# Kernel tuning notes

Measured on AMD Instinct MI355X. Metric: run time of the kernel, lower is better.

Reference implementation:

```python
import jax, jax.numpy as jnp
import numpy as np

N_ENT = 50000
N_REL = 16
N_BASES = 8
H_DIM = 128
N_EDGES = 800000


def setup_inputs() -> dict:
    key = jax.random.key(0)
    ks = jax.random.split(key, 12)
    s = 1.0 / np.sqrt(H_DIM)
    inp = {
        "entity_emb": jax.random.normal(ks[0], (N_ENT, H_DIM), jnp.float32) * s,
        "basis1": jax.random.normal(ks[1], (N_BASES, H_DIM, H_DIM), jnp.float32) * s,
        "w_comp1": jax.random.normal(ks[2], (N_REL, N_BASES), jnp.float32) * (1.0 / np.sqrt(N_BASES)),
        "loop_w1": jax.random.normal(ks[3], (H_DIM, H_DIM), jnp.float32) * s,
        "bias1": jnp.zeros((H_DIM,), jnp.float32),
        "basis2": jax.random.normal(ks[4], (N_BASES, H_DIM, H_DIM), jnp.float32) * s,
        "w_comp2": jax.random.normal(ks[5], (N_REL, N_BASES), jnp.float32) * (1.0 / np.sqrt(N_BASES)),
        "loop_w2": jax.random.normal(ks[6], (H_DIM, H_DIM), jnp.float32) * s,
        "bias2": jnp.zeros((H_DIM,), jnp.float32),
        "src": jax.random.randint(ks[7], (N_EDGES,), 0, N_ENT, jnp.int32),
        "dst": jax.random.randint(ks[8], (N_EDGES,), 0, N_ENT, jnp.int32),
        "rel_type": jax.random.randint(ks[9], (N_EDGES,), 0, N_REL, jnp.int32),
    }
    return inp


def _rgcn_layer(h, src, dst, rel, basis, w_comp, loop_w, bias):
    # Basis decomposition: W_r = sum_b w_comp[r, b] * basis[b]   -> [R, d, d]
    W = jnp.einsum('rb,bio->rio', w_comp, basis)
    # Sum aggregation is linear, so aggregate h[src] per (dst, rel) first,
    # then apply the relation matrix once per (node, rel). Same math as
    # per-edge transform + scatter-add, far less FLOP/traffic.
    seg = dst.astype(jnp.int32) * N_REL + rel.astype(jnp.int32)  # [E]
    agg = jax.ops.segment_sum(h[src], seg, num_segments=N_ENT * N_REL)
    agg = agg.reshape(N_ENT, N_REL, -1)                           # [N, R, d]
    msg = jnp.einsum('nri,rio->no', agg, W)                       # [N, d]
    out = msg + h @ loop_w + bias
    return jax.nn.relu(out)


def reference(entity_emb, basis1, w_comp1, loop_w1, bias1,
              basis2, w_comp2, loop_w2, bias2, src, dst, rel_type):
    # Encoder dropout is identity in eval mode.
    h = _rgcn_layer(entity_emb, src, dst, rel_type, basis1, w_comp1, loop_w1, bias1)
    h = _rgcn_layer(h, src, dst, rel_type, basis2, w_comp2, loop_w2, bias2)
    return h
```

## Files before the change

### kernel.cpp

```cpp
#include <hip/hip_runtime.h>
#include <hip/hip_bf16.h>

#define HDIM 128
#define NREL 16
#define NBASES 8
#define KSLOTS 17
#define KDIM (KSLOTS * HDIM)
#define LDSA 136

typedef short bf16x8 __attribute__((ext_vector_type(8)));
typedef short s16x4 __attribute__((ext_vector_type(4)));
typedef float f32x4 __attribute__((ext_vector_type(4)));

static __device__ __forceinline__ short f2bf(float x) {
    __hip_bfloat16 b = __float2bfloat16(x);
    return *(short*)&b;
}
static __device__ __forceinline__ float bf2f(short u) {
    unsigned v = ((unsigned)(unsigned short)u) << 16;
    return __uint_as_float(v);
}

__global__ void compute_wt(const float* __restrict__ basis,
                           const float* __restrict__ wcomp,
                           short* __restrict__ wtL) {
    int ro = blockIdx.x;
    int r = ro >> 7, o = ro & 127;
    int i = threadIdx.x;
    float acc = 0.f;
#pragma unroll
    for (int b = 0; b < NBASES; ++b)
        acc += wcomp[r * NBASES + b] * basis[(b * HDIM + i) * HDIM + o];
    wtL[(size_t)o * KDIM + r * HDIM + i] = f2bf(acc);
}

__global__ void transposeL(const float* __restrict__ in, short* __restrict__ wtL) {
    int o = blockIdx.x, i = threadIdx.x;
    wtL[(size_t)o * KDIM + NREL * HDIM + i] = f2bf(in[i * HDIM + o]);
}

__global__ void cast_bf16(const float* __restrict__ in, short* __restrict__ out, int n4) {
    for (int i = blockIdx.x * blockDim.x + threadIdx.x; i < n4; i += gridDim.x * blockDim.x) {
        f32x4 v = ((const f32x4*)in)[i];
        s16x4 o;
#pragma unroll
        for (int j = 0; j < 4; ++j) o[j] = f2bf(v[j]);
        ((s16x4*)out)[i] = o;
    }
}

__global__ void zero_i32(int* __restrict__ p, int n) {
    int i = blockIdx.x * blockDim.x + threadIdx.x;
    if (i < n) p[i] = 0;
}

__global__ __launch_bounds__(256) void hist_k(const int* __restrict__ dst,
                                              const int* __restrict__ rel, int n,
                                              int* __restrict__ hist) {
    for (int i = blockIdx.x * blockDim.x + threadIdx.x; i < n; i += gridDim.x * blockDim.x)
        atomicAdd(&hist[dst[i] * NREL + rel[i]], 1);
}

__global__ __launch_bounds__(1024) void scan_p1(const int* __restrict__ hist, int n,
                                                int* __restrict__ off, int* __restrict__ part) {
    __shared__ int sh[1024];
    int t = threadIdx.x, b = blockIdx.x;
    int i = b * 1024 + t;
    int x = (i < n) ? hist[i] : 0;
    sh[t] = x;
    __syncthreads();
    for (int d = 1; d < 1024; d <<= 1) {
        int v = sh[t];
        int u = (t >= d) ? sh[t - d] : 0;
        __syncthreads();
        sh[t] = v + u;
        __syncthreads();
    }
    if (i < n) off[i] = sh[t] - x;
    if (t == 1023) part[b] = sh[t];
}

__global__ __launch_bounds__(1024) void scan_p2(int* __restrict__ part, int nb) {
    __shared__ int sh[1024];
    int t = threadIdx.x;
    int x = (t < nb) ? part[t] : 0;
    sh[t] = x;
    __syncthreads();
    for (int d = 1; d < 1024; d <<= 1) {
        int v = sh[t];
        int u = (t >= d) ? sh[t - d] : 0;
        __syncthreads();
        sh[t] = v + u;
        __syncthreads();
    }
    if (t < nb) part[t] = sh[t] - x;
}

__global__ __launch_bounds__(1024) void scan_p3(int* __restrict__ off, const int* __restrict__ part,
                                                int n, int nk, int* __restrict__ cur) {
    int i = blockIdx.x * 1024 + threadIdx.x;
    if (i < n) {
        int v = off[i] + part[blockIdx.x];
        off[i] = v;
        if (i < nk) cur[i] = v;
    }
}

__global__ __launch_bounds__(256) void scatter_k(const int* __restrict__ src,
                                                 const int* __restrict__ dst,
                                                 const int* __restrict__ rel, int n,
                                                 int* __restrict__ cur,
                                                 int* __restrict__ edge2) {
    for (int i = blockIdx.x * blockDim.x + threadIdx.x; i < n; i += gridDim.x * blockDim.x) {
        int k = dst[i] * NREL + rel[i];
        int p = atomicAdd(&cur[k], 1);
        edge2[p] = (src[i] & 0xFFFF) | (rel[i] << 16);
    }
}

__global__ __launch_bounds__(256) void agg_build(
    const short* __restrict__ h,
    const int* __restrict__ off,
    const int* __restrict__ edge2,
    short* __restrict__ AGG,
    unsigned char* __restrict__ mask,
    int c0, int rows) {
    int tid = threadIdx.x;
    int grp = blockIdx.x * 16 + (tid >> 4);
    int lane16 = tid & 15;
    int lane = tid & 63;
    int gb = lane & 48;
    int drow = grp >> 1;
    if (drow >= rows) return;
    int rh = (grp & 1) * 8;
    int d = c0 + drow;
    int kbase = d * NREL + rh;

    int e0 = off[kbase];
    int e1 = off[kbase + 8];
    int deg = e1 - e0;

    int pkv = (e0 + lane16 < e1) ? edge2[e0 + lane16] : 0;

    bf16x8 va[16];
    int rlv[16];
#pragma unroll
    for (int p = 0; p < 16; ++p) {
        int pk = __shfl(pkv, gb + p);
        rlv[p] = ((pk >> 16) & 15) - rh;
        const short* hp = h + (size_t)(pk & 0xFFFF) * HDIM + lane16 * 8;
        if (p < deg) va[p] = *(const bf16x8*)hp;
    }

    float acc[8];
    int cs = -1;
    unsigned mbits = 0;
    short* outp = AGG + ((size_t)drow * NREL + rh) * HDIM + lane16 * 8;

    auto emit = [&]() {
        bf16x8 o;
#pragma unroll
        for (int c = 0; c < 8; ++c) o[c] = f2bf(acc[c]);
        *(bf16x8*)(outp + cs * HDIM) = o;
        mbits |= 1u << cs;
    };
    auto take = [&](int sl, bf16x8 v) {
        if (sl != cs) {
            if (cs >= 0) emit();
            cs = sl;
#pragma unroll
            for (int c = 0; c < 8; ++c) acc[c] = 0.f;
        }
#pragma unroll
        for (int c = 0; c < 8; ++c) acc[c] += bf2f(v[c]);
    };

#pragma unroll
    for (int p = 0; p < 16; ++p)
        if (p < deg) take(rlv[p], va[p]);

    for (int e = e0 + 16; e < e1; ++e) {
        int pk = edge2[e];
        bf16x8 v = *(const bf16x8*)(h + (size_t)(pk & 0xFFFF) * HDIM + lane16 * 8);
        take(((pk >> 16) & 15) - rh, v);
    }
    if (cs >= 0) emit();

    if (lane16 == 0) mask[(size_t)drow * 2 + (rh >> 3)] = (unsigned char)mbits;
}

__global__ __launch_bounds__(256, 3) void agg_gemm(
    const short* __restrict__ AGG,
    const short* __restrict__ h,
    const short* __restrict__ wtL,
    const unsigned char* __restrict__ mask,
    const float* __restrict__ bias,
    short* __restrict__ out_bf,
    float* __restrict__ out_f,
    int c0, int rows) {
    __shared__ short As[64 * LDSA];
    __shared__ short Bs[128 * LDSA];
    int tid = threadIdx.x;
    int row0 = blockIdx.x * 64;
    if (row0 >= rows) return;
    int wave = tid >> 6, lane = tid & 63;
    int mq = (wave & 1) * 32, nq = (wave >> 1) * 64;
    int lr = lane & 15, quad = lane >> 4;

    int r2 = tid >> 2, ch = (tid & 3) * 32;
    int rb = tid >> 1, hb = (tid & 1) * 64;
    bool ok = (row0 + r2) < rows;
    unsigned mk = ok ? *(const unsigned short*)(mask + (size_t)(row0 + r2) * 2) : 0;

    bf16x8 apf[4], bpf[8];

    auto loadRegs = [&](int ks) {
        const short* bp = wtL + (size_t)rb * KDIM + ks * HDIM + hb;
#pragma unroll
        for (int j = 0; j < 8; ++j) bpf[j] = *(const bf16x8*)(bp + j * 8);
        if (ks == 16) {
            const short* sp = h + (size_t)(c0 + row0 + r2) * HDIM + ch;
#pragma unroll
            for (int j = 0; j < 4; ++j) apf[j] = ok ? *(const bf16x8*)(sp + j * 8) : (bf16x8)0;
        } else if (ok && ((mk >> ks) & 1)) {
            const short* sp = AGG + ((size_t)(row0 + r2) * NREL + ks) * HDIM + ch;
#pragma unroll
            for (int j = 0; j < 4; ++j) apf[j] = *(const bf16x8*)(sp + j * 8);
        } else {
#pragma unroll
            for (int j = 0; j < 4; ++j) apf[j] = (bf16x8)0;
        }
    };
    auto writeLDS = [&]() {
        short* ad = As + r2 * LDSA + ch;
#pragma unroll
        for (int j = 0; j < 4; ++j) *(bf16x8*)(ad + j * 8) = apf[j];
        short* bd = Bs + rb * LDSA + hb;
#pragma unroll
        for (int j = 0; j < 8; ++j) *(bf16x8*)(bd + j * 8) = bpf[j];
    };

    f32x4 acc[2][4] = {};

    loadRegs(0);
    writeLDS();
    __syncthreads();

#pragma unroll 1
    for (int ks = 0; ks <= 16; ++ks) {
        if (ks < 16) loadRegs(ks + 1);
#pragma unroll
        for (int kk = 0; kk < 4; ++kk) {
            int kb = kk * 32 + quad * 8;
            bf16x8 a[2], b[4];
#pragma unroll
            for (int mi = 0; mi < 2; ++mi)
                a[mi] = *(const bf16x8*)(As + (mq + mi * 16 + lr) * LDSA + kb);
#pragma unroll
            for (int ni = 0; ni < 4; ++ni)
                b[ni] = *(const bf16x8*)(Bs + (nq + ni * 16 + lr) * LDSA + kb);
#pragma unroll
            for (int mi = 0; mi < 2; ++mi)
#pragma unroll
                for (int ni = 0; ni < 4; ++ni)
                    acc[mi][ni] = __builtin_amdgcn_mfma_f32_16x16x32_bf16(a[mi], b[ni], acc[mi][ni], 0, 0, 0);
        }
        __syncthreads();
        if (ks < 16) { writeLDS(); __syncthreads(); }
    }

#pragma unroll
    for (int mi = 0; mi < 2; ++mi) {
#pragma unroll
        for (int reg = 0; reg < 4; ++reg) {
            int g = row0 + mq + mi * 16 + quad * 4 + reg;
            if (g < rows) {
                size_t gd = (size_t)(c0 + g) * HDIM;
#pragma unroll
                for (int ni = 0; ni < 4; ++ni) {
                    int n = nq + ni * 16 + lr;
                    float v = acc[mi][ni][reg] + bias[n];
                    v = v > 0.f ? v : 0.f;
                    if (out_bf) out_bf[gd + n] = f2bf(v);
                    else        out_f[gd + n] = v;
                }
            }
        }
    }
}

extern "C" void kernel_launch(void* const* d_in, const int* in_sizes, int n_in,
                              void* d_out, int out_size, void* d_ws, size_t ws_size,
                              hipStream_t stream) {
    const float* emb    = (const float*)d_in[0];
    const float* basis1 = (const float*)d_in[1];
    const float* wc1    = (const float*)d_in[2];
    const float* lw1    = (const float*)d_in[3];
    const float* bias1  = (const float*)d_in[4];
    const float* basis2 = (const float*)d_in[5];
    const float* wc2    = (const float*)d_in[6];
    const float* lw2    = (const float*)d_in[7];
    const float* bias2  = (const float*)d_in[8];
    const int* src = (const int*)d_in[9];
    const int* dst = (const int*)d_in[10];
    const int* rel = (const int*)d_in[11];

    int n_ent = in_sizes[0] / HDIM;
    int n_edges = in_sizes[9];
    int NK = n_ent * NREL;
    int NK1 = NK + 1;

    char* ws = (char*)d_ws;
    size_t wo = 0;
    auto alloc = [&](size_t bytes) {
        void* p = ws + wo;
        wo = (wo + bytes + 255) & ~(size_t)255;
        return p;
    };
    int* hist  = (int*)alloc((size_t)NK1 * 4);
    int* off   = (int*)alloc((size_t)NK1 * 4);
    int* cur   = (int*)alloc((size_t)NK * 4);
    int* part  = (int*)alloc(4096);
    int* edge2 = (int*)alloc((size_t)n_edges * 4);
    short* wtL1 = (short*)alloc((size_t)HDIM * KDIM * 2);
    short* wtL2 = (short*)alloc((size_t)HDIM * KDIM * 2);
    short* h0   = (short*)alloc((size_t)n_ent * HDIM * 2);
    short* h1   = (short*)alloc((size_t)n_ent * HDIM * 2);
    unsigned char* mask = (unsigned char*)alloc((size_t)n_ent * 2);

    size_t rowBytes = (size_t)NREL * HDIM * 2;
    size_t avail = (ws_size > wo + rowBytes * 128) ? (ws_size - wo) : rowBytes * 128;
    int CH = (int)(avail / rowBytes);
    if (CH > n_ent) CH = n_ent;
    CH = (CH + 127) & ~127;
    if (CH < 128) CH = 128;
    while ((size_t)CH * rowBytes > avail && CH > 128) CH -= 128;
    short* AGG = (short*)alloc((size_t)CH * rowBytes);

    compute_wt<<<NREL * HDIM, HDIM, 0, stream>>>(basis1, wc1, wtL1);
    compute_wt<<<NREL * HDIM, HDIM, 0, stream>>>(basis2, wc2, wtL2);
    transposeL<<<HDIM, HDIM, 0, stream>>>(lw1, wtL1);
    transposeL<<<HDIM, HDIM, 0, stream>>>(lw2, wtL2);
    cast_bf16<<<512, 256, 0, stream>>>(emb, h0, n_ent * HDIM / 4);

    zero_i32<<<(NK1 + 255) / 256, 256, 0, stream>>>(hist, NK1);
    hist_k<<<1024, 256, 0, stream>>>(dst, rel, n_edges, hist);
    int nsb = (NK1 + 1023) / 1024;
    scan_p1<<<nsb, 1024, 0, stream>>>(hist, NK1, off, part);
    scan_p2<<<1, 1024, 0, stream>>>(part, nsb);
    scan_p3<<<nsb, 1024, 0, stream>>>(off, part, NK1, NK, cur);
    scatter_k<<<1024, 256, 0, stream>>>(src, dst, rel, n_edges, cur, edge2);

    for (int c0 = 0; c0 < n_ent; c0 += CH) {
        int rows = n_ent - c0 < CH ? n_ent - c0 : CH;
        agg_build<<<(rows * 2 + 15) / 16, 256, 0, stream>>>(h0, off, edge2, AGG, mask, c0, rows);
        agg_gemm<<<(rows + 63) / 64, 256, 0, stream>>>(AGG, h0, wtL1, mask, bias1,
                                                       h1, nullptr, c0, rows);
    }
    for (int c0 = 0; c0 < n_ent; c0 += CH) {
        int rows = n_ent - c0 < CH ? n_ent - c0 : CH;
        agg_build<<<(rows * 2 + 15) / 16, 256, 0, stream>>>(h1, off, edge2, AGG, mask, c0, rows);
        agg_gemm<<<(rows + 63) / 64, 256, 0, stream>>>(AGG, h1, wtL2, mask, bias2,
                                                       nullptr, (float*)d_out, c0, rows);
    }
}
```

Before: 502.3 us.

## Skip materializing single-edge aggregates; read source rows directly in GEMM, swizzle LDS

agg_build now detects (dst, rel) slots that hold exactly one edge and, instead of summing and writing them to AGG, records the source node index in a per-slot srcs array. Multi-edge slots are marked with a sentinel and still go through AGG, and empty slots get a different sentinel. agg_gemm reads the slot descriptor and loads the A tile either from AGG, directly from h, or as zeros. This cuts AGG write and read traffic, since most slots in the random graph have degree one. The padded LDS layout is also replaced with an XOR-swizzled unpadded layout to avoid bank conflicts, which adds index arithmetic and a larger per-row srcs array.

```diff
diff --git a/kernel.cpp b/kernel.cpp
--- a/kernel.cpp
+++ b/kernel.cpp
@@ -6,7 +6,6 @@
 #define NBASES 8
 #define KSLOTS 17
 #define KDIM (KSLOTS * HDIM)
-#define LDSA 136
 
 typedef short bf16x8 __attribute__((ext_vector_type(8)));
 typedef short s16x4 __attribute__((ext_vector_type(4)));
@@ -123,7 +122,7 @@
     const int* __restrict__ off,
     const int* __restrict__ edge2,
     short* __restrict__ AGG,
-    unsigned char* __restrict__ mask,
+    unsigned short* __restrict__ srcs,
     int c0, int rows) {
     int tid = threadIdx.x;
     int grp = blockIdx.x * 16 + (tid >> 4);
@@ -137,24 +136,39 @@
     int kbase = d * NREL + rh;
 
     int e0 = off[kbase];
-    int e1 = off[kbase + 8];
-    int deg = e1 - e0;
-
-    int pkv = (e0 + lane16 < e1) ? edge2[e0 + lane16] : 0;
-
-    bf16x8 va[16];
-    int rlv[16];
+    int e8 = off[kbase + 8];
+    int deg = e8 - e0;
+
+    int pkv = (e0 + lane16 < e8) ? edge2[e0 + lane16] : 0;
+
+    int rlv[17], srcv[16];
 #pragma unroll
     for (int p = 0; p < 16; ++p) {
         int pk = __shfl(pkv, gb + p);
-        rlv[p] = ((pk >> 16) & 15) - rh;
-        const short* hp = h + (size_t)(pk & 0xFFFF) * HDIM + lane16 * 8;
-        if (p < deg) va[p] = *(const bf16x8*)hp;
-    }
-
-    float acc[8];
+        rlv[p] = (p < deg) ? (((pk >> 16) & 15) - rh) : 255;
+        srcv[p] = pk & 0xFFFF;
+    }
+    rlv[16] = (deg > 16) ? rlv[15] : 255;
+
+    bool single[16];
+#pragma unroll
+    for (int p = 0; p < 16; ++p)
+        single[p] = ((p == 0) || (rlv[p - 1] != rlv[p])) && (rlv[p + 1] != rlv[p]);
+
+    bf16x8 va[16];
+#pragma unroll
+    for (int p = 0; p < 16; ++p)
+        if (p < deg && !single[p])
+            va[p] = *(const bf16x8*)(h + (size_t)srcv[p] * HDIM + lane16 * 8);
+
+    unsigned short val = 0xFFFF;
+#pragma unroll
+    for (int p = 0; p < 16; ++p)
+        if (p < deg && rlv[p] == lane16)
+            val = single[p] ? (unsigned short)srcv[p] : (unsigned short)0xFFFE;
+
+    float acc[8] = {0.f, 0.f, 0.f, 0.f, 0.f, 0.f, 0.f, 0.f};
     int cs = -1;
-    unsigned mbits = 0;
     short* outp = AGG + ((size_t)drow * NREL + rh) * HDIM + lane16 * 8;
 
     auto emit = [&]() {
@@ -162,7 +176,6 @@
 #pragma unroll
         for (int c = 0; c < 8; ++c) o[c] = f2bf(acc[c]);
         *(bf16x8*)(outp + cs * HDIM) = o;
-        mbits |= 1u << cs;
     };
     auto take = [&](int sl, bf16x8 v) {
         if (sl != cs) {
@@ -177,29 +190,31 @@
 
 #pragma unroll
     for (int p = 0; p < 16; ++p)
-        if (p < deg) take(rlv[p], va[p]);
-
-    for (int e = e0 + 16; e < e1; ++e) {
+        if (p < deg && !single[p]) take(rlv[p], va[p]);
+
+    for (int e = e0 + 16; e < e8; ++e) {
         int pk = edge2[e];
+        int sl = ((pk >> 16) & 15) - rh;
+        if (sl == lane16) val = 0xFFFE;
         bf16x8 v = *(const bf16x8*)(h + (size_t)(pk & 0xFFFF) * HDIM + lane16 * 8);
-        take(((pk >> 16) & 15) - rh, v);
+        take(sl, v);
     }
     if (cs >= 0) emit();
 
-    if (lane16 == 0) mask[(size_t)drow * 2 + (rh >> 3)] = (unsigned char)mbits;
+    if (lane16 < 8) srcs[(size_t)drow * NREL + rh + lane16] = val;
 }
 
 __global__ __launch_bounds__(256, 3) void agg_gemm(
     const short* __restrict__ AGG,
     const short* __restrict__ h,
     const short* __restrict__ wtL,
-    const unsigned char* __restrict__ mask,
+    const unsigned short* __restrict__ srcs,
     const float* __restrict__ bias,
     short* __restrict__ out_bf,
     float* __restrict__ out_f,
     int c0, int rows) {
-    __shared__ short As[64 * LDSA];
-    __shared__ short Bs[128 * LDSA];
+    __shared__ short As[64 * HDIM];
+    __shared__ short Bs[128 * HDIM];
     int tid = threadIdx.x;
     int row0 = blockIdx.x * 64;
     if (row0 >= rows) return;
@@ -207,37 +222,64 @@
     int mq = (wave & 1) * 32, nq = (wave >> 1) * 64;
     int lr = lane & 15, quad = lane >> 4;
 
-    int r2 = tid >> 2, ch = (tid & 3) * 32;
-    int rb = tid >> 1, hb = (tid & 1) * 64;
+    int r2 = tid >> 2, ca = tid & 3;
+    int rb = tid >> 1, cb = (tid & 1) * 8;
     bool ok = (row0 + r2) < rows;
-    unsigned mk = ok ? *(const unsigned short*)(mask + (size_t)(row0 + r2) * 2) : 0;
+
+    unsigned wq[8];
+    {
+        uint4 a = make_uint4(0xFFFFFFFFu, 0xFFFFFFFFu, 0xFFFFFFFFu, 0xFFFFFFFFu);
+        uint4 b = a;
+        if (ok) {
+            const uint4* sp = (const uint4*)(srcs + (size_t)(row0 + r2) * NREL);
+            a = sp[0]; b = sp[1];
+        }
+        wq[0] = a.x; wq[1] = a.y; wq[2] = a.z; wq[3] = a.w;
+        wq[4] = b.x; wq[5] = b.y; wq[6] = b.z; wq[7] = b.w;
+    }
 
     bf16x8 apf[4], bpf[8];
-
     auto loadRegs = [&](int ks) {
-        const short* bp = wtL + (size_t)rb * KDIM + ks * HDIM + hb;
+        const short* bp = wtL + (size_t)rb * KDIM + ks * HDIM + cb * 8;
 #pragma unroll
         for (int j = 0; j < 8; ++j) bpf[j] = *(const bf16x8*)(bp + j * 8);
         if (ks == 16) {
-            const short* sp = h + (size_t)(c0 + row0 + r2) * HDIM + ch;
-#pragma unroll
-            for (int j = 0; j < 4; ++j) apf[j] = ok ? *(const bf16x8*)(sp + j * 8) : (bf16x8)0;
-        } else if (ok && ((mk >> ks) & 1)) {
-            const short* sp = AGG + ((size_t)(row0 + r2) * NREL + ks) * HDIM + ch;
-#pragma unroll
-            for (int j = 0; j < 4; ++j) apf[j] = *(const bf16x8*)(sp + j * 8);
+            if (ok) {
+                const short* sp = h + (size_t)(c0 + row0 + r2) * HDIM + ca * 32;
+#pragma unroll
+                for (int j = 0; j < 4; ++j) apf[j] = *(const bf16x8*)(sp + j * 8);
+            } else {
+#pragma unroll
+                for (int j = 0; j < 4; ++j) apf[j] = (bf16x8)0;
+            }
         } else {
-#pragma unroll
-            for (int j = 0; j < 4; ++j) apf[j] = (bf16x8)0;
+            unsigned w = 0xFFFFu;
+#pragma unroll
+            for (int q = 0; q < 8; ++q) if ((ks >> 1) == q) w = wq[q];
+            unsigned e = (ks & 1) ? (w >> 16) : (w & 0xFFFFu);
+            if (e == 0xFFFFu) {
+#pragma unroll
+                for (int j = 0; j < 4; ++j) apf[j] = (bf16x8)0;
+            } else {
+                const short* sp = (e == 0xFFFEu)
+                    ? AGG + ((size_t)(row0 + r2) * NREL + ks) * HDIM + ca * 32
+                    : h + (size_t)e * HDIM + ca * 32;
+#pragma unroll
+                for (int j = 0; j < 4; ++j) apf[j] = *(const bf16x8*)(sp + j * 8);
+            }
         }
     };
     auto writeLDS = [&]() {
-        short* ad = As + r2 * LDSA + ch;
-#pragma unroll
-        for (int j = 0; j < 4; ++j) *(bf16x8*)(ad + j * 8) = apf[j];
-        short* bd = Bs + rb * LDSA + hb;
-#pragma unroll
-        for (int j = 0; j < 8; ++j) *(bf16x8*)(bd + j * 8) = bpf[j];
+#pragma unroll
+        for (int j = 0; j < 4; ++j) {
+            int c = ca * 4 + j;
+            *(bf16x8*)(As + r2 * HDIM + (c ^ (r2 & 7)) * 8) = apf[j];
+        }
+#pragma unroll
+        for (int j = 0; j < 8; ++j) {
+            int c = cb + j;
+            *(bf16x8*)(Bs + rb * HDIM + (c ^ (rb & 7)) * 8) = bpf[j];
+        }
     };
 
     f32x4 acc[2][4] = {};
@@ -251,14 +293,18 @@
         if (ks < 16) loadRegs(ks + 1);
 #pragma unroll
         for (int kk = 0; kk < 4; ++kk) {
-            int kb = kk * 32 + quad * 8;
+            int c = kk * 4 + quad;
             bf16x8 a[2], b[4];
 #pragma unroll
-            for (int mi = 0; mi < 2; ++mi)
-                a[mi] = *(const bf16x8*)(As + (mq + mi * 16 + lr) * LDSA + kb);
-#pragma unroll
-            for (int ni = 0; ni < 4; ++ni)
-                b[ni] = *(const bf16x8*)(Bs + (nq + ni * 16 + lr) * LDSA + kb);
+            for (int mi = 0; mi < 2; ++mi) {
+                int row = mq + mi * 16 + lr;
+                a[mi] = *(const bf16x8*)(As + row * HDIM + (c ^ (row & 7)) * 8);
+            }
+#pragma unroll
+            for (int ni = 0; ni < 4; ++ni) {
+                int row = nq + ni * 16 + lr;
+                b[ni] = *(const bf16x8*)(Bs + row * HDIM + (c ^ (row & 7)) * 8);
+            }
 #pragma unroll
             for (int mi = 0; mi < 2; ++mi)
 #pragma unroll
@@ -326,7 +372,7 @@
     short* wtL2 = (short*)alloc((size_t)HDIM * KDIM * 2);
     short* h0   = (short*)alloc((size_t)n_ent * HDIM * 2);
     short* h1   = (short*)alloc((size_t)n_ent * HDIM * 2);
-    unsigned char* mask = (unsigned char*)alloc((size_t)n_ent * 2);
+    unsigned short* srcs = (unsigned short*)alloc((size_t)n_ent * NREL * 2);
 
     size_t rowBytes = (size_t)NREL * HDIM * 2;
     size_t avail = (ws_size > wo + rowBytes * 128) ? (ws_size - wo) : rowBytes * 128;
@@ -353,14 +399,14 @@
 
     for (int c0 = 0; c0 < n_ent; c0 += CH) {
         int rows = n_ent - c0 < CH ? n_ent - c0 : CH;
-        agg_build<<<(rows * 2 + 15) / 16, 256, 0, stream>>>(h0, off, edge2, AGG, mask, c0, rows);
-        agg_gemm<<<(rows + 63) / 64, 256, 0, stream>>>(AGG, h0, wtL1, mask, bias1,
+        agg_build<<<(rows * 2 + 15) / 16, 256, 0, stream>>>(h0, off, edge2, AGG, srcs, c0, rows);
+        agg_gemm<<<(rows + 63) / 64, 256, 0, stream>>>(AGG, h0, wtL1, srcs, bias1,
                                                        h1, nullptr, c0, rows);
     }
     for (int c0 = 0; c0 < n_ent; c0 += CH) {
         int rows = n_ent - c0 < CH ? n_ent - c0 : CH;
-        agg_build<<<(rows * 2 + 15) / 16, 256, 0, stream>>>(h1, off, edge2, AGG, mask, c0, rows);
-        agg_gemm<<<(rows + 63) / 64, 256, 0, stream>>>(AGG, h1, wtL2, mask, bias2,
+        agg_build<<<(rows * 2 + 15) / 16, 256, 0, stream>>>(h1, off, edge2, AGG, srcs, c0, rows);
+        agg_gemm<<<(rows + 63) / 64, 256, 0, stream>>>(AGG, h1, wtL2, srcs, bias2,
                                                        nullptr, (float*)d_out, c0, rows);
     }
 }
```

Result: faster. 490.8 us (-2.3%).

## Compact aggregation buffer: store only multi-edge segments, reference single-edge sources directly

Applied to the files above, without the earlier changes.

Replaces the dense per-(node,relation) AGG buffer with a compacted buffer holding only segments of degree two or more, indexed through a second thresholded prefix scan. Single-edge segments store the source node index so the GEMM loads the h row directly, and empty segments are marked so their A tile is zeroed. This shrinks AGG write and read traffic and removes the chunked loop over entities, at the cost of an extra scan pass and indirect per-slot address selection in the GEMM.

```diff
diff --git a/kernel.cpp b/kernel.cpp
--- a/kernel.cpp
+++ b/kernel.cpp
@@ -62,11 +62,13 @@
 }
 
 __global__ __launch_bounds__(1024) void scan_p1(const int* __restrict__ hist, int n,
-                                                int* __restrict__ off, int* __restrict__ part) {
+                                                int* __restrict__ off, int* __restrict__ part,
+                                                int thr) {
     __shared__ int sh[1024];
     int t = threadIdx.x, b = blockIdx.x;
     int i = b * 1024 + t;
     int x = (i < n) ? hist[i] : 0;
+    if (thr) x = (x >= thr) ? 1 : 0;
     sh[t] = x;
     __syncthreads();
     for (int d = 1; d < 1024; d <<= 1) {
@@ -121,10 +123,11 @@
 __global__ __launch_bounds__(256) void agg_build(
     const short* __restrict__ h,
     const int* __restrict__ off,
+    const int* __restrict__ off2m,
     const int* __restrict__ edge2,
-    short* __restrict__ AGG,
-    unsigned char* __restrict__ mask,
-    int c0, int rows) {
+    short* __restrict__ AGGc,
+    unsigned* __restrict__ srcs,
+    int rows) {
     int tid = threadIdx.x;
     int grp = blockIdx.x * 16 + (tid >> 4);
     int lane16 = tid & 15;
@@ -133,36 +136,56 @@
     int drow = grp >> 1;
     if (drow >= rows) return;
     int rh = (grp & 1) * 8;
-    int d = c0 + drow;
-    int kbase = d * NREL + rh;
-
-    int e0 = off[kbase];
-    int e1 = off[kbase + 8];
-    int deg = e1 - e0;
-
-    int pkv = (e0 + lane16 < e1) ? edge2[e0 + lane16] : 0;
-
-    bf16x8 va[16];
-    int rlv[16];
+    int kbase = drow * NREL + rh;
+
+    int offv = (lane16 < 9) ? off[kbase + lane16] : 0;
+    int cmv  = (lane16 < 8) ? off2m[kbase + lane16] : 0;
+    int e0 = __shfl(offv, gb);
+    int e8 = __shfl(offv, gb + 8);
+    int deg = e8 - e0;
+    int nl = gb + ((lane16 < 8) ? lane16 + 1 : 0);
+    int degS = __shfl(offv, nl) - offv;
+
+    int pkv = (e0 + lane16 < e8) ? edge2[e0 + lane16] : 0;
+    int rlv[16], srcv[16], mul[16];
 #pragma unroll
     for (int p = 0; p < 16; ++p) {
         int pk = __shfl(pkv, gb + p);
-        rlv[p] = ((pk >> 16) & 15) - rh;
-        const short* hp = h + (size_t)(pk & 0xFFFF) * HDIM + lane16 * 8;
-        if (p < deg) va[p] = *(const bf16x8*)hp;
-    }
-
-    float acc[8];
+        int sl = ((pk >> 16) & 15) - rh;
+        rlv[p] = (p < deg) ? sl : 0;
+        srcv[p] = pk & 0xFFFF;
+        int ds = __shfl(degS, gb + rlv[p]);
+        mul[p] = (p < deg) && (ds >= 2);
+    }
+
+    bf16x8 va[16];
+#pragma unroll
+    for (int p = 0; p < 16; ++p)
+        if (mul[p])
+            va[p] = *(const bf16x8*)(h + (size_t)srcv[p] * HDIM + lane16 * 8);
+
+    unsigned val = 0xFFFFFFFFu;
+    if (lane16 < 8) {
+        if (degS >= 2) val = 0x80000000u | (unsigned)cmv;
+        else if (degS == 1) {
+            int ps = offv - e0;
+            if (ps < 16) {
+#pragma unroll
+                for (int p = 0; p < 16; ++p) if (ps == p) val = (unsigned)srcv[p];
+            } else {
+                val = (unsigned)(edge2[e0 + ps] & 0xFFFF);
+            }
+        }
+    }
+
+    float acc[8] = {0.f, 0.f, 0.f, 0.f, 0.f, 0.f, 0.f, 0.f};
     int cs = -1;
-    unsigned mbits = 0;
-    short* outp = AGG + ((size_t)drow * NREL + rh) * HDIM + lane16 * 8;
-
     auto emit = [&]() {
+        int cmS = __shfl(cmv, gb + cs);
         bf16x8 o;
 #pragma unroll
         for (int c = 0; c < 8; ++c) o[c] = f2bf(acc[c]);
-        *(bf16x8*)(outp + cs * HDIM) = o;
-        mbits |= 1u << cs;
+        *(bf16x8*)(AGGc + (size_t)cmS * HDIM + lane16 * 8) = o;
     };
     auto take = [&](int sl, bf16x8 v) {
         if (sl != cs) {
@@ -177,27 +200,31 @@
 
 #pragma unroll
     for (int p = 0; p < 16; ++p)
-        if (p < deg) take(rlv[p], va[p]);
-
-    for (int e = e0 + 16; e < e1; ++e) {
+        if (mul[p]) take(rlv[p], va[p]);
+
+    for (int e = e0 + 16; e < e8; ++e) {
         int pk = edge2[e];
-        bf16x8 v = *(const bf16x8*)(h + (size_t)(pk & 0xFFFF) * HDIM + lane16 * 8);
-        take(((pk >> 16) & 15) - rh, v);
+        int sl = ((pk >> 16) & 15) - rh;
+        int ds = __shfl(degS, gb + sl);
+        if (ds >= 2) {
+            bf16x8 v = *(const bf16x8*)(h + (size_t)(pk & 0xFFFF) * HDIM + lane16 * 8);
+            take(sl, v);
+        }
     }
     if (cs >= 0) emit();
 
-    if (lane16 == 0) mask[(size_t)drow * 2 + (rh >> 3)] = (unsigned char)mbits;
+    if (lane16 < 8) srcs[(size_t)drow * NREL + rh + lane16] = val;
 }
 
 __global__ __launch_bounds__(256, 3) void agg_gemm(
-    const short* __restrict__ AGG,
+    const short* __restrict__ AGGc,
     const short* __restrict__ h,
     const short* __restrict__ wtL,
-    const unsigned char* __restrict__ mask,
+    const unsigned* __restrict__ srcs,
     const float* __restrict__ bias,
     short* __restrict__ out_bf,
     float* __restrict__ out_f,
-    int c0, int rows) {
+    int rows) {
     __shared__ short As[64 * LDSA];
     __shared__ short Bs[128 * LDSA];
     int tid = threadIdx.x;
@@ -207,32 +234,50 @@
     int mq = (wave & 1) * 32, nq = (wave >> 1) * 64;
     int lr = lane & 15, quad = lane >> 4;
 
-    int r2 = tid >> 2, ch = (tid & 3) * 32;
+    int r2 = tid >> 2, ca = (tid & 3) * 32;
     int rb = tid >> 1, hb = (tid & 1) * 64;
     bool ok = (row0 + r2) < rows;
-    unsigned mk = ok ? *(const unsigned short*)(mask + (size_t)(row0 + r2) * 2) : 0;
+
+    unsigned cq[16];
+    {
+        uint4 f4 = make_uint4(0xFFFFFFFFu, 0xFFFFFFFFu, 0xFFFFFFFFu, 0xFFFFFFFFu);
+        uint4 v0 = f4, v1 = f4, v2 = f4, v3 = f4;
+        if (ok) {
+            const uint4* p = (const uint4*)(srcs + (size_t)(row0 + r2) * NREL);
+            v0 = p[0]; v1 = p[1]; v2 = p[2]; v3 = p[3];
+        }
+        cq[0] = v0.x; cq[1] = v0.y; cq[2] = v0.z; cq[3] = v0.w;
+        cq[4] = v1.x; cq[5] = v1.y; cq[6] = v1.z; cq[7] = v1.w;
+        cq[8] = v2.x; cq[9] = v2.y; cq[10] = v2.z; cq[11] = v2.w;
+        cq[12] = v3.x; cq[13] = v3.y; cq[14] = v3.z; cq[15] = v3.w;
+    }
 
     bf16x8 apf[4], bpf[8];
-
     auto loadRegs = [&](int ks) {
         const short* bp = wtL + (size_t)rb * KDIM + ks * HDIM + hb;
 #pragma unroll
         for (int j = 0; j < 8; ++j) bpf[j] = *(const bf16x8*)(bp + j * 8);
+        unsigned e;
         if (ks == 16) {
-            const short* sp = h + (size_t)(c0 + row0 + r2) * HDIM + ch;
-#pragma unroll
-            for (int j = 0; j < 4; ++j) apf[j] = ok ? *(const bf16x8*)(sp + j * 8) : (bf16x8)0;
-        } else if (ok && ((mk >> ks) & 1)) {
-            const short* sp = AGG + ((size_t)(row0 + r2) * NREL + ks) * HDIM + ch;
+            e = ok ? (unsigned)(row0 + r2) : 0xFFFFFFFFu;
+        } else {
+            e = 0xFFFFFFFFu;
+#pragma unroll
+            for (int q = 0; q < 16; ++q) if (ks == q) e = cq[q];
+        }
+        if (e == 0xFFFFFFFFu) {
+#pragma unroll
+            for (int j = 0; j < 4; ++j) apf[j] = (bf16x8)0;
+        } else {
+            const short* sp = (e & 0x80000000u)
+                ? AGGc + (size_t)(e & 0x7FFFFFFFu) * HDIM + ca
+                : h + (size_t)e * HDIM + ca;
 #pragma unroll
             for (int j = 0; j < 4; ++j) apf[j] = *(const bf16x8*)(sp + j * 8);
-        } else {
-#pragma unroll
-            for (int j = 0; j < 4; ++j) apf[j] = (bf16x8)0;
         }
     };
     auto writeLDS = [&]() {
-        short* ad = As + r2 * LDSA + ch;
+        short* ad = As + r2 * LDSA + ca;
 #pragma unroll
         for (int j = 0; j < 4; ++j) *(bf16x8*)(ad + j * 8) = apf[j];
         short* bd = Bs + rb * LDSA + hb;
@@ -252,18 +297,18 @@
 #pragma unroll
         for (int kk = 0; kk < 4; ++kk) {
             int kb = kk * 32 + quad * 8;
-            bf16x8 a[2], b[4];
+            bf16x8 a2[2], b4[4];
 #pragma unroll
             for (int mi = 0; mi < 2; ++mi)
-                a[mi] = *(const bf16x8*)(As + (mq + mi * 16 + lr) * LDSA + kb);
+                a2[mi] = *(const bf16x8*)(As + (mq + mi * 16 + lr) * LDSA + kb);
 #pragma unroll
             for (int ni = 0; ni < 4; ++ni)
-                b[ni] = *(const bf16x8*)(Bs + (nq + ni * 16 + lr) * LDSA + kb);
+                b4[ni] = *(const bf16x8*)(Bs + (nq + ni * 16 + lr) * LDSA + kb);
 #pragma unroll
             for (int mi = 0; mi < 2; ++mi)
 #pragma unroll
                 for (int ni = 0; ni < 4; ++ni)
-                    acc[mi][ni] = __builtin_amdgcn_mfma_f32_16x16x32_bf16(a[mi], b[ni], acc[mi][ni], 0, 0, 0);
+                    acc[mi][ni] = __builtin_amdgcn_mfma_f32_16x16x32_bf16(a2[mi], b4[ni], acc[mi][ni], 0, 0, 0);
         }
         __syncthreads();
         if (ks < 16) { writeLDS(); __syncthreads(); }
@@ -275,7 +320,7 @@
         for (int reg = 0; reg < 4; ++reg) {
             int g = row0 + mq + mi * 16 + quad * 4 + reg;
             if (g < rows) {
-                size_t gd = (size_t)(c0 + g) * HDIM;
+                size_t gd = (size_t)g * HDIM;
 #pragma unroll
                 for (int ni = 0; ni < 4; ++ni) {
                     int n = nq + ni * 16 + lr;
@@ -317,25 +362,21 @@
         wo = (wo + bytes + 255) & ~(size_t)255;
         return p;
     };
-    int* hist  = (int*)alloc((size_t)NK1 * 4);
-    int* off   = (int*)alloc((size_t)NK1 * 4);
-    int* cur   = (int*)alloc((size_t)NK * 4);
-    int* part  = (int*)alloc(4096);
-    int* edge2 = (int*)alloc((size_t)n_edges * 4);
+    int* hist   = (int*)alloc((size_t)NK1 * 4);
+    int* off    = (int*)alloc((size_t)NK1 * 4);
+    int* off2m  = (int*)alloc((size_t)NK1 * 4);
+    int* cur    = (int*)alloc((size_t)NK * 4);
+    int* part   = (int*)alloc(4096);
+    int* edge2  = (int*)alloc((size_t)n_edges * 4);
     short* wtL1 = (short*)alloc((size_t)HDIM * KDIM * 2);
     short* wtL2 = (short*)alloc((size_t)HDIM * KDIM * 2);
     short* h0   = (short*)alloc((size_t)n_ent * HDIM * 2);
     short* h1   = (short*)alloc((size_t)n_ent * HDIM * 2);
-    unsigned char* mask = (unsigned char*)alloc((size_t)n_ent * 2);
-
-    size_t rowBytes = (size_t)NREL * HDIM * 2;
-    size_t avail = (ws_size > wo + rowBytes * 128) ? (ws_size - wo) : rowBytes * 128;
-    int CH = (int)(avail / rowBytes);
-    if (CH > n_ent) CH = n_ent;
-    CH = (CH + 127) & ~127;
-    if (CH < 128) CH = 128;
-    while ((size_t)CH * rowBytes > avail && CH > 128) CH -= 128;
-    short* AGG = (short*)alloc((size_t)CH * rowBytes);
+    unsigned* srcs = (unsigned*)alloc((size_t)n_ent * NREL * 4);
+    size_t aggMax = (size_t)(n_edges / 2 + 64) * HDIM * 2;
+    size_t remain = (ws_size > wo) ? ws_size - wo : 0;
+    if (aggMax > remain) aggMax = remain;
+    short* AGGc = (short*)alloc(aggMax);
 
     compute_wt<<<NREL * HDIM, HDIM, 0, stream>>>(basis1, wc1, wtL1);
     compute_wt<<<NREL * HDIM, HDIM, 0, stream>>>(basis2, wc2, wtL2);
@@ -346,21 +387,19 @@
     zero_i32<<<(NK1 + 255) / 256, 256, 0, stream>>>(hist, NK1);
     hist_k<<<1024, 256, 0, stream>>>(dst, rel, n_edges, hist);
     int nsb = (NK1 + 1023) / 1024;
-    scan_p1<<<nsb, 1024, 0, stream>>>(hist, NK1, off, part);
+    scan_p1<<<nsb, 1024, 0, stream>>>(hist, NK1, off, part, 0);
     scan_p2<<<1, 1024, 0, stream>>>(part, nsb);
     scan_p3<<<nsb, 1024, 0, stream>>>(off, part, NK1, NK, cur);
     scatter_k<<<1024, 256, 0, stream>>>(src, dst, rel, n_edges, cur, edge2);
-
-    for (int c0 = 0; c0 < n_ent; c0 += CH) {
-        int rows = n_ent - c0 < CH ? n_ent - c0 : CH;
-        agg_build<<<(rows * 2 + 15) / 16, 256, 0, stream>>>(h0, off, edge2, AGG, mask, c0, rows);
-        agg_gemm<<<(rows + 63) / 64, 256, 0, stream>>>(AGG, h0, wtL1, mask, bias1,
-                                                       h1, nullptr, c0, rows);
-    }
-    for (int c0 = 0; c0 < n_ent; c0 += CH) {
-        int rows = n_ent - c0 < CH ? n_ent - c0 : CH;
-        agg_build<<<(rows * 2 + 15) / 16, 256, 0, stream>>>(h1, off, edge2, AGG, mask, c0, rows);
-        agg_gemm<<<(rows + 63) / 64, 256, 0, stream>>>(AGG, h1, wtL2, mask, bias2,
-                                                       nullptr, (float*)d_out, c0, rows);
-    }
-}
+    scan_p1<<<nsb, 1024, 0, stream>>>(hist, NK1, off2m, part, 2);
+    scan_p2<<<1, 1024, 0, stream>>>(part, nsb);
+    scan_p3<<<nsb, 1024, 0, stream>>>(off2m, part, NK1, 0, cur);
+
+    int btiles = (n_ent * 2 + 15) / 16;
+    int gtiles = (n_ent + 63) / 64;
+
+    agg_build<<<btiles, 256, 0, stream>>>(h0, off, off2m, edge2, AGGc, srcs, n_ent);
+    agg_gemm<<<gtiles, 256, 0, stream>>>(AGGc, h0, wtL1, srcs, bias1, h1, nullptr, n_ent);
+    agg_build<<<btiles, 256, 0, stream>>>(h1, off, off2m, edge2, AGGc, srcs, n_ent);
+    agg_gemm<<<gtiles, 256, 0, stream>>>(AGGc, h1, wtL2, srcs, bias2, nullptr, (float*)d_out, n_ent);
+}
```

Result: no change. 504.3 us (+0.4%).
